# Kernel optimization log

Measured on AMD Instinct MI355X. Metric: run time of the kernel, lower is better.

The kernel has to match this reference:

```python
import jax, jax.numpy as jnp
import numpy as np

N, E = 50000, 800000
D_IN, D_HID, D_OUT = 128, 128, 64
BN_EPS = 1e-5
GEN_EPS = 1e-7


def _lin_init(k, fan_in, shape):
    lim = 1.0 / np.sqrt(fan_in)
    return jax.random.uniform(k, shape, minval=-lim, maxval=lim, dtype=jnp.float32)


def setup_inputs() -> dict:
    key = jax.random.key(0)
    ks = jax.random.split(key, 12)
    x = jax.random.normal(ks[0], (N, D_IN), dtype=jnp.float32)
    edge_index = jax.random.randint(ks[1], (2, E), 0, N, dtype=jnp.int64)
    return {
        "x": x,
        # GCNConv 0 and 1 (Glorot-ish uniform init like PyG Linear)
        "W0": _lin_init(ks[2], D_IN, (D_IN, D_HID)), "b0": jnp.zeros((D_HID,), jnp.float32),
        "g0": jnp.ones((D_HID,), jnp.float32), "beta0": jnp.zeros((D_HID,), jnp.float32),
        "W1": _lin_init(ks[3], D_HID, (D_HID, D_HID)), "b1": jnp.zeros((D_HID,), jnp.float32),
        "g1": jnp.ones((D_HID,), jnp.float32), "beta1": jnp.zeros((D_HID,), jnp.float32),
        # GENConv MLP: [D_HID] -> [2*D_HID] (BN+ReLU) -> [D_OUT]
        "Wg1": _lin_init(ks[4], D_HID, (D_HID, 2 * D_HID)), "bg1": jnp.zeros((2 * D_HID,), jnp.float32),
        "gg": jnp.ones((2 * D_HID,), jnp.float32), "betag": jnp.zeros((2 * D_HID,), jnp.float32),
        "Wg2": _lin_init(ks[5], 2 * D_HID, (2 * D_HID, D_OUT)), "bg2": jnp.zeros((D_OUT,), jnp.float32),
        "edge_index": edge_index,
    }


def _bn(h, gamma, beta):
    # BatchNorm1d, training-mode batch statistics (biased variance)
    mu = jnp.mean(h, axis=0)
    var = jnp.mean(jnp.square(h - mu), axis=0)
    return (h - mu) * jax.lax.rsqrt(var + BN_EPS) * gamma + beta


def _gcn_conv(x, W, b, src, dst, n):
    # GCNConv: D^-1/2 (A + I) D^-1/2 (x W) + b
    loop = jnp.arange(n, dtype=src.dtype)
    s = jnp.concatenate([src, loop])
    d = jnp.concatenate([dst, loop])
    deg = jax.ops.segment_sum(jnp.ones_like(s, dtype=x.dtype), d, num_segments=n)
    dinv = jax.lax.rsqrt(deg)  # deg >= 1 due to self-loops
    norm = dinv[s] * dinv[d]   # [E+N]
    h = x @ W                  # [N, D]
    agg = jax.ops.segment_sum(norm[:, None] * h[s], d, num_segments=n)
    return agg + b


def _gen_conv(x, W1, b1, g, beta, W2, b2, src, dst, n):
    # GENConv (defaults): msg = relu(x_j) + eps; per-channel softmax aggregation
    # (t=1); residual add of x_dst; then MLP [D, 2D (BN+ReLU), D_out].
    msg = jax.nn.relu(x[src]) + GEN_EPS            # [E, D]
    m = jax.ops.segment_max(msg, dst, num_segments=n)
    m = jnp.where(jnp.isfinite(m), m, 0.0)         # guard zero in-degree nodes
    ex = jnp.exp(msg - m[dst])                     # [E, D]
    denom = jax.ops.segment_sum(ex, dst, num_segments=n)
    num = jax.ops.segment_sum(ex * msg, dst, num_segments=n)
    agg = num / jnp.maximum(denom, 1e-16)          # [N, D]
    out = agg + x                                  # residual
    h = jax.nn.relu(_bn(out @ W1 + b1, g, beta))
    return h @ W2 + b2


def reference(x, W0, b0, g0, beta0, W1, b1, g1, beta1,
              Wg1, bg1, gg, betag, Wg2, bg2, edge_index):
    src, dst = edge_index[0], edge_index[1]
    n = x.shape[0]
    # layer 0: GCNConv -> BN -> ReLU (dropout is identity in eval)
    h = _gcn_conv(x, W0, b0, src, dst, n)
    h = jax.nn.relu(_bn(h, g0, beta0))
    # layer 1
    h = _gcn_conv(h, W1, b1, src, dst, n)
    h = jax.nn.relu(_bn(h, g1, beta1))
    # final GENConv + log-softmax over classes
    h = _gen_conv(h, Wg1, bg1, gg, betag, Wg2, bg2, src, dst, n)
    return jax.nn.log_softmax(h, axis=-1)
```

## Files before the change

### kernel.cpp

```cpp
#include <hip/hip_runtime.h>
#include <hip/hip_bf16.h>

#define DIN 128
#define DHID 128
#define DCLS 64
#define BN_EPS 1e-5f
#define GEN_EPS 1e-7f

typedef __attribute__((ext_vector_type(8))) short short8;
typedef __attribute__((ext_vector_type(4))) float f32x4;

static __device__ __forceinline__ float bf2f(unsigned short u) {
    union { float f; unsigned int i; } x; x.i = ((unsigned int)u) << 16; return x.f;
}
static __device__ __forceinline__ unsigned short f2bf(float f) {
    union { float f; unsigned int i; } x; x.f = f;
    unsigned int r = x.i + 0x7fffu + ((x.i >> 16) & 1u);
    return (unsigned short)(r >> 16);
}
static __device__ __forceinline__ float bflo(unsigned int u) {
    union { float f; unsigned int i; } x; x.i = u << 16; return x.f;
}
static __device__ __forceinline__ float bfhi(unsigned int u) {
    union { float f; unsigned int i; } x; x.i = u & 0xffff0000u; return x.f;
}
static __device__ __forceinline__ unsigned int packbf(float lo, float hi) {
    return ((unsigned int)f2bf(hi) << 16) | f2bf(lo);
}

__global__ void k_hist(const int* __restrict__ dst, int* __restrict__ counts, int E) {
    int e = blockIdx.x * 256 + threadIdx.x;
    if (e < E) atomicAdd(&counts[dst[e]], 1);
}

__global__ __launch_bounds__(256) void k_scan1(const int* __restrict__ counts,
        int* __restrict__ roff, int* __restrict__ bsum, int N) {
    __shared__ int ls[256];
    int t = threadIdx.x;
    int base = blockIdx.x * 1024 + t * 4;
    int c0 = 0, c1 = 0, c2 = 0, c3 = 0;
    if (base + 3 < N) {
        int4 v = *(const int4*)(counts + base);
        c0 = v.x; c1 = v.y; c2 = v.z; c3 = v.w;
    } else {
        if (base + 0 < N) c0 = counts[base + 0];
        if (base + 1 < N) c1 = counts[base + 1];
        if (base + 2 < N) c2 = counts[base + 2];
        if (base + 3 < N) c3 = counts[base + 3];
    }
    ls[t] = c0 + c1 + c2 + c3;
    __syncthreads();
    for (int off = 1; off < 256; off <<= 1) {
        int v = (t >= off) ? ls[t - off] : 0;
        __syncthreads();
        ls[t] += v;
        __syncthreads();
    }
    int r = (t == 0) ? 0 : ls[t - 1];
    if (base + 0 < N) { roff[base + 0] = r; r += c0; }
    if (base + 1 < N) { roff[base + 1] = r; r += c1; }
    if (base + 2 < N) { roff[base + 2] = r; r += c2; }
    if (base + 3 < N) { roff[base + 3] = r; }
    if (t == 255) bsum[blockIdx.x] = ls[255];
}

__global__ __launch_bounds__(1024) void k_scan2(int* __restrict__ bsum, int nblk) {
    __shared__ int ls[1024];
    int t = threadIdx.x;
    ls[t] = (t < nblk) ? bsum[t] : 0;
    __syncthreads();
    for (int off = 1; off < 1024; off <<= 1) {
        int v = (t >= off) ? ls[t - off] : 0;
        __syncthreads();
        ls[t] += v;
        __syncthreads();
    }
    if (t < nblk) bsum[t] = (t == 0) ? 0 : ls[t - 1];
}

__global__ void k_scan3(const int* __restrict__ counts, const int* __restrict__ bsum,
        int* __restrict__ roff, int* __restrict__ cursor, float* __restrict__ dinv,
        int N, int E) {
    int i = blockIdx.x * 256 + threadIdx.x;
    if (i < N) {
        int r = roff[i] + bsum[i >> 10];
        roff[i] = r; cursor[i] = r;
        dinv[i] = rsqrtf((float)(counts[i] + 1));
    }
    if (i == 0) roff[N] = E;
}

__global__ void k_fill(const int* __restrict__ src, const int* __restrict__ dst,
        int* __restrict__ cursor, int* __restrict__ srcs, int E) {
    int e = blockIdx.x * 256 + threadIdx.x;
    if (e < E) {
        int d = dst[e];
        int p = atomicAdd(&cursor[d], 1);
        srcs[p] = src[e];
    }
}

__global__ void k_wt(const float* __restrict__ W, unsigned short* __restrict__ Wt, int K, int Dout) {
    int i = blockIdx.x * 256 + threadIdx.x;
    if (i >= K * Dout) return;
    int n = i / K, k = i - n * K;
    Wt[i] = f2bf(W[(size_t)k * Dout + n]);
}

template<int K, bool ABF16, bool OBF16>
__global__ __launch_bounds__(256) void k_gemm(const void* __restrict__ Av,
        const unsigned short* __restrict__ Wt, const float* __restrict__ bias,
        const float* __restrict__ scale, const float* __restrict__ shift,
        const float* __restrict__ rowscale,
        void* __restrict__ Cv, int nrows, int Dout) {
    constexpr int KP = K + 8;
    __shared__ unsigned short sA[64 * KP];
    __shared__ unsigned short sW[64 * KP];
    const int tid = threadIdx.x;
    const int row0 = blockIdx.x * 64, col0 = blockIdx.y * 64;

#pragma unroll
    for (int it = 0; it < (64 * K) / (256 * 4); ++it) {
        int idx = (it * 256 + tid) * 4;
        int r = idx / K, c = idx % K;
        int gr = row0 + r;
        float v0 = 0.f, v1 = 0.f, v2 = 0.f, v3 = 0.f;
        if (gr < nrows) {
            if (ABF16) {
                ushort4 u = *(const ushort4*)((const unsigned short*)Av + (size_t)gr * K + c);
                v0 = bf2f(u.x); v1 = bf2f(u.y); v2 = bf2f(u.z); v3 = bf2f(u.w);
            } else {
                float4 f = *(const float4*)((const float*)Av + (size_t)gr * K + c);
                v0 = f.x; v1 = f.y; v2 = f.z; v3 = f.w;
            }
            if (scale) {
                v0 = fmaxf(v0 * scale[c + 0] + shift[c + 0], 0.f);
                v1 = fmaxf(v1 * scale[c + 1] + shift[c + 1], 0.f);
                v2 = fmaxf(v2 * scale[c + 2] + shift[c + 2], 0.f);
                v3 = fmaxf(v3 * scale[c + 3] + shift[c + 3], 0.f);
            }
        }
        ushort4 o; o.x = f2bf(v0); o.y = f2bf(v1); o.z = f2bf(v2); o.w = f2bf(v3);
        *(ushort4*)(&sA[r * KP + c]) = o;
    }
#pragma unroll
    for (int it = 0; it < (64 * K) / (256 * 8); ++it) {
        int idx = (it * 256 + tid) * 8;
        int r = idx / K, c = idx % K;
        uint4 u = *(const uint4*)(Wt + (size_t)(col0 + r) * K + c);
        *(uint4*)(&sW[r * KP + c]) = u;
    }
    __syncthreads();

    const int w = tid >> 6, lane = tid & 63;
    const int wr = (w >> 1) * 32, wc = (w & 1) * 32;
    const int lr = lane & 15, kg = (lane >> 4) * 8;
    f32x4 acc[2][2] = {};
#pragma unroll
    for (int kk = 0; kk < K; kk += 32) {
        short8 af[2], bfr[2];
#pragma unroll
        for (int mi = 0; mi < 2; mi++)
            af[mi] = *(const short8*)(&sA[(wr + mi * 16 + lr) * KP + kk + kg]);
#pragma unroll
        for (int ni = 0; ni < 2; ni++)
            bfr[ni] = *(const short8*)(&sW[(wc + ni * 16 + lr) * KP + kk + kg]);
#pragma unroll
        for (int mi = 0; mi < 2; mi++)
#pragma unroll
            for (int ni = 0; ni < 2; ni++)
                acc[mi][ni] = __builtin_amdgcn_mfma_f32_16x16x32_bf16(af[mi], bfr[ni], acc[mi][ni], 0, 0, 0);
    }
#pragma unroll
    for (int mi = 0; mi < 2; mi++) {
#pragma unroll
        for (int ni = 0; ni < 2; ni++) {
            int r = wr + mi * 16 + (lane >> 4) * 4;
            int cgl = col0 + wc + ni * 16 + (lane & 15);
            float bv = bias ? bias[cgl] : 0.f;
#pragma unroll
            for (int j = 0; j < 4; j++) {
                int gr = row0 + r + j;
                if (gr < nrows) {
                    float val = acc[mi][ni][j] + bv;
                    if (rowscale) val *= rowscale[gr];
                    if (OBF16) ((unsigned short*)Cv)[(size_t)gr * Dout + cgl] = f2bf(val);
                    else       ((float*)Cv)[(size_t)gr * Dout + cgl] = val;
                }
            }
        }
    }
}

__global__ __launch_bounds__(256) void k_gcn_agg(const unsigned short* __restrict__ p,
        const int* __restrict__ roff, const int* __restrict__ srcs,
        const float* __restrict__ dinv, const float* __restrict__ b,
        unsigned short* __restrict__ out, int N) {
    int nw = (gridDim.x * 256) >> 6;
    int wid = (blockIdx.x * 256 + threadIdx.x) >> 6;
    int lane = threadIdx.x & 63;
    int q = lane >> 4, l16 = lane & 15;
    int c = l16 * 8;
    float4 bl = *(const float4*)(b + c);
    float4 bh = *(const float4*)(b + c + 4);
    for (int d = wid; d < N; d += nw) {
        float a0=0.f,a1=0.f,a2=0.f,a3=0.f,a4=0.f,a5=0.f,a6=0.f,a7=0.f;
        int e0 = roff[d], e1 = roff[d + 1];
        for (int e = e0 + q; e < e1; e += 4) {
            int s = srcs[e];
            uint4 u = ((const uint4*)(p + (size_t)s * 128))[l16];
            a0 += bflo(u.x); a1 += bfhi(u.x);
            a2 += bflo(u.y); a3 += bfhi(u.y);
            a4 += bflo(u.z); a5 += bfhi(u.z);
            a6 += bflo(u.w); a7 += bfhi(u.w);
        }
        if (q == 0) {
            uint4 u = ((const uint4*)(p + (size_t)d * 128))[l16];
            a0 += bflo(u.x); a1 += bfhi(u.x);
            a2 += bflo(u.y); a3 += bfhi(u.y);
            a4 += bflo(u.z); a5 += bfhi(u.z);
            a6 += bflo(u.w); a7 += bfhi(u.w);
        }
        a0 += __shfl_xor(a0,16); a0 += __shfl_xor(a0,32);
        a1 += __shfl_xor(a1,16); a1 += __shfl_xor(a1,32);
        a2 += __shfl_xor(a2,16); a2 += __shfl_xor(a2,32);
        a3 += __shfl_xor(a3,16); a3 += __shfl_xor(a3,32);
        a4 += __shfl_xor(a4,16); a4 += __shfl_xor(a4,32);
        a5 += __shfl_xor(a5,16); a5 += __shfl_xor(a5,32);
        a6 += __shfl_xor(a6,16); a6 += __shfl_xor(a6,32);
        a7 += __shfl_xor(a7,16); a7 += __shfl_xor(a7,32);
        if (q == 0) {
            float dv = dinv[d];
            uint4 o;
            o.x = packbf(dv*a0 + bl.x, dv*a1 + bl.y);
            o.y = packbf(dv*a2 + bl.z, dv*a3 + bl.w);
            o.z = packbf(dv*a4 + bh.x, dv*a5 + bh.y);
            o.w = packbf(dv*a6 + bh.z, dv*a7 + bh.w);
            ((uint4*)(out + (size_t)d * 128))[l16] = o;
        }
    }
}

__global__ __launch_bounds__(256) void k_gen_agg(const unsigned short* __restrict__ t4,
        const int* __restrict__ roff, const int* __restrict__ srcs,
        const float* __restrict__ scale, const float* __restrict__ shift,
        unsigned short* __restrict__ out, int N) {
    int nw = (gridDim.x * 256) >> 6;
    int wid = (blockIdx.x * 256 + threadIdx.x) >> 6;
    int lane = threadIdx.x & 63;
    int q = lane >> 4, l16 = lane & 15;
    int c = l16 * 8;
    float4 scl = *(const float4*)(scale + c);
    float4 sch = *(const float4*)(scale + c + 4);
    float4 shl = *(const float4*)(shift + c);
    float4 shh = *(const float4*)(shift + c + 4);
    float sc[8] = {scl.x, scl.y, scl.z, scl.w, sch.x, sch.y, sch.z, sch.w};
    float sh[8] = {shl.x, shl.y, shl.z, shl.w, shh.x, shh.y, shh.z, shh.w};
    for (int d = wid; d < N; d += nw) {
        float de[8] = {0,0,0,0,0,0,0,0};
        float nu[8] = {0,0,0,0,0,0,0,0};
        int e0 = roff[d], e1 = roff[d + 1];
        for (int e = e0 + q; e < e1; e += 4) {
            int s = srcs[e];
            uint4 u = ((const uint4*)(t4 + (size_t)s * 128))[l16];
            float v[8] = {bflo(u.x), bfhi(u.x), bflo(u.y), bfhi(u.y),
                          bflo(u.z), bfhi(u.z), bflo(u.w), bfhi(u.w)};
#pragma unroll
            for (int k = 0; k < 8; k++) {
                float m = fmaxf(v[k] * sc[k] + sh[k], 0.f) + GEN_EPS;
                float w = __expf(fminf(m, 80.f));
                de[k] += w; nu[k] += w * m;
            }
        }
#pragma unroll
        for (int k = 0; k < 8; k++) {
            de[k] += __shfl_xor(de[k],16); de[k] += __shfl_xor(de[k],32);
            nu[k] += __shfl_xor(nu[k],16); nu[k] += __shfl_xor(nu[k],32);
        }
        if (q == 0) {
            uint4 u = ((const uint4*)(t4 + (size_t)d * 128))[l16];
            float v[8] = {bflo(u.x), bfhi(u.x), bflo(u.y), bfhi(u.y),
                          bflo(u.z), bfhi(u.z), bflo(u.w), bfhi(u.w)};
            float r[8];
            bool has = (e1 > e0);
#pragma unroll
            for (int k = 0; k < 8; k++) {
                float h2 = fmaxf(v[k] * sc[k] + sh[k], 0.f);
                float a = has ? nu[k] / de[k] : 0.f;
                r[k] = a + h2;
            }
            uint4 o;
            o.x = packbf(r[0], r[1]); o.y = packbf(r[2], r[3]);
            o.z = packbf(r[4], r[5]); o.w = packbf(r[6], r[7]);
            ((uint4*)(out + (size_t)d * 128))[l16] = o;
        }
    }
}

template<int D>
__global__ __launch_bounds__(256) void k_stats(const unsigned short* __restrict__ h,
        float* __restrict__ gsum, float* __restrict__ gsq, int N) {
    constexpr int HC = D / 2, TPC = 256 / HC;
    int t = threadIdx.x;
    int cp = t % HC, slot = t / HC;
    int c = cp * 2;
    float s0 = 0.f, s1 = 0.f, q0 = 0.f, q1 = 0.f;
    for (int node = blockIdx.x * TPC + slot; node < N; node += gridDim.x * TPC) {
        ushort2 u = *(const ushort2*)(h + (size_t)node * D + c);
        float v0 = bf2f(u.x), v1 = bf2f(u.y);
        s0 += v0; s1 += v1; q0 += v0 * v0; q1 += v1 * v1;
    }
    __shared__ float red[256 * 4];
    red[t * 4] = s0; red[t * 4 + 1] = s1; red[t * 4 + 2] = q0; red[t * 4 + 3] = q1;
    __syncthreads();
    if (slot == 0) {
        for (int k2 = 1; k2 < TPC; k2++) {
            int o = (t + k2 * HC) * 4;
            s0 += red[o]; s1 += red[o + 1]; q0 += red[o + 2]; q1 += red[o + 3];
        }
        atomicAdd(&gsum[c], s0); atomicAdd(&gsum[c + 1], s1);
        atomicAdd(&gsq[c], q0); atomicAdd(&gsq[c + 1], q1);
    }
}

__global__ void k_fin(const float* __restrict__ sum, const float* __restrict__ sq,
        const float* __restrict__ g, const float* __restrict__ beta,
        float* __restrict__ scale, float* __restrict__ shift, int D, float invN) {
    int c = threadIdx.x;
    if (c < D) {
        float mu = sum[c] * invN;
        float var = sq[c] * invN - mu * mu;
        float s = g[c] * rsqrtf(var + BN_EPS);
        scale[c] = s;
        shift[c] = beta[c] - mu * s;
    }
}

__global__ __launch_bounds__(256) void k_head(float* __restrict__ out, int N) {
    int wid = blockIdx.x * 4 + (threadIdx.x >> 6);
    int lane = threadIdx.x & 63;
    if (wid >= N) return;
    float v = out[(size_t)wid * 64 + lane];
    float m = v;
    for (int o = 32; o; o >>= 1) m = fmaxf(m, __shfl_xor(m, o));
    float e = __expf(v - m);
    float s = e;
    for (int o = 32; o; o >>= 1) s += __shfl_xor(s, o);
    out[(size_t)wid * 64 + lane] = v - m - __logf(s);
}

extern "C" void kernel_launch(void* const* d_in, const int* in_sizes, int n_in,
                              void* d_out, int out_size, void* d_ws, size_t ws_size,
                              hipStream_t stream) {
    const float* x   = (const float*)d_in[0];
    const float* W0  = (const float*)d_in[1];
    const float* b0  = (const float*)d_in[2];
    const float* g0  = (const float*)d_in[3];
    const float* be0 = (const float*)d_in[4];
    const float* W1  = (const float*)d_in[5];
    const float* b1  = (const float*)d_in[6];
    const float* g1  = (const float*)d_in[7];
    const float* be1 = (const float*)d_in[8];
    const float* Wg1 = (const float*)d_in[9];
    const float* bg1 = (const float*)d_in[10];
    const float* gg  = (const float*)d_in[11];
    const float* beg = (const float*)d_in[12];
    const float* Wg2 = (const float*)d_in[13];
    const float* bg2 = (const float*)d_in[14];
    const int*   ei  = (const int*)d_in[15];

    const int N = in_sizes[0] / DIN;
    const int E = in_sizes[15] / 2;
    const int* src = ei;
    const int* dst = ei + E;

    char* ws = (char*)d_ws;
    size_t off = 0;
    auto alloc = [&](size_t b) { size_t o = off; off = (off + b + 255) & ~(size_t)255; return o; };
    size_t o_counts = alloc((size_t)N * 4);
    size_t o_stats  = alloc(1024 * 4);
    size_t o_cursor = alloc((size_t)N * 4);
    size_t o_roff   = alloc(((size_t)N + 1) * 4);
    size_t o_srcs   = alloc((size_t)E * 4);
    size_t o_dinv   = alloc((size_t)N * 4);
    size_t o_bsum   = alloc(1024 * 4);
    size_t o_ss     = alloc(1024 * 4);
    size_t o_w0t    = alloc(128 * 128 * 2);
    size_t o_w1t    = alloc(128 * 128 * 2);
    size_t o_wg1t   = alloc(256 * 128 * 2);
    size_t o_wg2t   = alloc(64 * 256 * 2);
    size_t o_xa     = alloc((size_t)N * 128 * 2);
    size_t o_xb     = alloc((size_t)N * 128 * 2);
    size_t o_c      = alloc((size_t)N * 256 * 2);
    (void)ws_size; (void)n_in; (void)out_size;

    int* counts = (int*)(ws + o_counts);
    float* stats = (float*)(ws + o_stats);
    int* cursor = (int*)(ws + o_cursor);
    int* roff = (int*)(ws + o_roff);
    int* srcs = (int*)(ws + o_srcs);
    float* dinv = (float*)(ws + o_dinv);
    int* bsum = (int*)(ws + o_bsum);
    float* ssz = (float*)(ws + o_ss);
    unsigned short* w0t  = (unsigned short*)(ws + o_w0t);
    unsigned short* w1t  = (unsigned short*)(ws + o_w1t);
    unsigned short* wg1t = (unsigned short*)(ws + o_wg1t);
    unsigned short* wg2t = (unsigned short*)(ws + o_wg2t);
    unsigned short* xa = (unsigned short*)(ws + o_xa);
    unsigned short* xb = (unsigned short*)(ws + o_xb);
    unsigned short* cb = (unsigned short*)(ws + o_c);

    float* sum0 = stats;       float* sq0 = stats + 128;
    float* sum1 = stats + 256; float* sq1 = stats + 384;
    float* sumg = stats + 512; float* sqg = stats + 768;
    float* scale0 = ssz;       float* shift0 = ssz + 128;
    float* scale1 = ssz + 256; float* shift1 = ssz + 384;
    float* scaleg = ssz + 512; float* shiftg = ssz + 768;

    hipMemsetAsync(ws + o_counts, 0, o_cursor - o_counts, stream);

    int egrid = (E + 255) / 256;
    int nblk = (N + 1023) / 1024;
    k_hist<<<egrid, 256, 0, stream>>>(dst, counts, E);
    k_scan1<<<nblk, 256, 0, stream>>>(counts, roff, bsum, N);
    k_scan2<<<1, 1024, 0, stream>>>(bsum, nblk);
    k_scan3<<<(N + 255) / 256, 256, 0, stream>>>(counts, bsum, roff, cursor, dinv, N, E);
    k_fill<<<egrid, 256, 0, stream>>>(src, dst, cursor, srcs, E);

    k_wt<<<(128 * 128 + 255) / 256, 256, 0, stream>>>(W0, w0t, 128, 128);
    k_wt<<<(128 * 128 + 255) / 256, 256, 0, stream>>>(W1, w1t, 128, 128);
    k_wt<<<(128 * 256 + 255) / 256, 256, 0, stream>>>(Wg1, wg1t, 128, 256);
    k_wt<<<(256 * 64 + 255) / 256, 256, 0, stream>>>(Wg2, wg2t, 256, 64);

    int rb = (N + 63) / 64;
    const float invN = 1.f / (float)N;

    k_gemm<128, false, true><<<dim3(rb, 2), 256, 0, stream>>>(x, w0t, nullptr, nullptr, nullptr, dinv, xa, N, 128);
    k_gcn_agg<<<2048, 256, 0, stream>>>(xa, roff, srcs, dinv, b0, xb, N);
    k_stats<128><<<1024, 256, 0, stream>>>(xb, sum0, sq0, N);
    k_fin<<<1, 256, 0, stream>>>(sum0, sq0, g0, be0, scale0, shift0, 128, invN);

    k_gemm<128, true, true><<<dim3(rb, 2), 256, 0, stream>>>(xb, w1t, nullptr, scale0, shift0, dinv, xa, N, 128);
    k_gcn_agg<<<2048, 256, 0, stream>>>(xa, roff, srcs, dinv, b1, xb, N);
    k_stats<128><<<1024, 256, 0, stream>>>(xb, sum1, sq1, N);
    k_fin<<<1, 256, 0, stream>>>(sum1, sq1, g1, be1, scale1, shift1, 128, invN);

    k_gen_agg<<<2048, 256, 0, stream>>>(xb, roff, srcs, scale1, shift1, xa, N);

    k_gemm<128, true, true><<<dim3(rb, 4), 256, 0, stream>>>(xa, wg1t, bg1, nullptr, nullptr, nullptr, cb, N, 256);
    k_stats<256><<<1024, 256, 0, stream>>>(cb, sumg, sqg, N);
    k_fin<<<1, 256, 0, stream>>>(sumg, sqg, gg, beg, scaleg, shiftg, 256, invN);
    k_gemm<256, true, false><<<dim3(rb, 1), 256, 0, stream>>>(cb, wg2t, bg2, scaleg, shiftg, nullptr, d_out, N, 64);

    k_head<<<(N + 3) / 4, 256, 0, stream>>>((float*)d_out, N);
}
```

Measured before the change: 524.8 us.

## Fuse BN stats into GCN aggregation and precompute per-node softmax weights

The GCN aggregation kernel now accumulates per-channel sum and sum-of-squares of its output and atomically adds them to global stats, replacing two separate k_stats passes over the node features. A new k_genpre kernel computes exp(m) and exp(m)*m once per node into a bf16 table (reusing the cb buffer). k_gen_agg then gathers these precomputed values instead of recomputing the BN affine, ReLU and exp for every edge. This doubles the bytes gathered per edge in the GEN aggregation and adds bf16 rounding of the weights, while removing per-edge transcendental work. Dropping the segment max is safe here only because the exponent is clamped at 80.

```diff
diff --git a/kernel.cpp b/kernel.cpp
--- a/kernel.cpp
+++ b/kernel.cpp
@@ -195,7 +195,8 @@
 __global__ __launch_bounds__(256) void k_gcn_agg(const unsigned short* __restrict__ p,
         const int* __restrict__ roff, const int* __restrict__ srcs,
         const float* __restrict__ dinv, const float* __restrict__ b,
-        unsigned short* __restrict__ out, int N) {
+        unsigned short* __restrict__ out,
+        float* __restrict__ gsum, float* __restrict__ gsq, int N) {
     int nw = (gridDim.x * 256) >> 6;
     int wid = (blockIdx.x * 256 + threadIdx.x) >> 6;
     int lane = threadIdx.x & 63;
@@ -203,6 +204,9 @@
     int c = l16 * 8;
     float4 bl = *(const float4*)(b + c);
     float4 bh = *(const float4*)(b + c + 4);
+    float bb[8] = {bl.x, bl.y, bl.z, bl.w, bh.x, bh.y, bh.z, bh.w};
+    float ls[8] = {0,0,0,0,0,0,0,0};
+    float lq[8] = {0,0,0,0,0,0,0,0};
     for (int d = wid; d < N; d += nw) {
         float a0=0.f,a1=0.f,a2=0.f,a3=0.f,a4=0.f,a5=0.f,a6=0.f,a7=0.f;
         int e0 = roff[d], e1 = roff[d + 1];
@@ -231,17 +235,73 @@
         a7 += __shfl_xor(a7,16); a7 += __shfl_xor(a7,32);
         if (q == 0) {
             float dv = dinv[d];
+            float r0 = dv*a0 + bb[0], r1 = dv*a1 + bb[1];
+            float r2 = dv*a2 + bb[2], r3 = dv*a3 + bb[3];
+            float r4 = dv*a4 + bb[4], r5 = dv*a5 + bb[5];
+            float r6 = dv*a6 + bb[6], r7 = dv*a7 + bb[7];
+            ls[0]+=r0; lq[0]+=r0*r0; ls[1]+=r1; lq[1]+=r1*r1;
+            ls[2]+=r2; lq[2]+=r2*r2; ls[3]+=r3; lq[3]+=r3*r3;
+            ls[4]+=r4; lq[4]+=r4*r4; ls[5]+=r5; lq[5]+=r5*r5;
+            ls[6]+=r6; lq[6]+=r6*r6; ls[7]+=r7; lq[7]+=r7*r7;
             uint4 o;
-            o.x = packbf(dv*a0 + bl.x, dv*a1 + bl.y);
-            o.y = packbf(dv*a2 + bl.z, dv*a3 + bl.w);
-            o.z = packbf(dv*a4 + bh.x, dv*a5 + bh.y);
-            o.w = packbf(dv*a6 + bh.z, dv*a7 + bh.w);
+            o.x = packbf(r0, r1); o.y = packbf(r2, r3);
+            o.z = packbf(r4, r5); o.w = packbf(r6, r7);
             ((uint4*)(out + (size_t)d * 128))[l16] = o;
         }
     }
+    __shared__ float sred[4][128];
+    __shared__ float qred[4][128];
+    int wv = threadIdx.x >> 6;
+    if (q == 0) {
+#pragma unroll
+        for (int k = 0; k < 8; k++) { sred[wv][c + k] = ls[k]; qred[wv][c + k] = lq[k]; }
+    }
+    __syncthreads();
+    int t = threadIdx.x;
+    if (t < 128) {
+        float s = sred[0][t] + sred[1][t] + sred[2][t] + sred[3][t];
+        float qq = qred[0][t] + qred[1][t] + qred[2][t] + qred[3][t];
+        atomicAdd(&gsum[t], s);
+        atomicAdd(&gsq[t], qq);
+    }
+}
+
+__global__ __launch_bounds__(256) void k_genpre(const unsigned short* __restrict__ t4,
+        const float* __restrict__ scale, const float* __restrict__ shift,
+        unsigned short* __restrict__ wt, int N) {
+    int i = blockIdx.x * 256 + threadIdx.x;
+    int node = i >> 4, l16 = i & 15;
+    if (node >= N) return;
+    int c = l16 * 8;
+    float4 scl = *(const float4*)(scale + c);
+    float4 sch = *(const float4*)(scale + c + 4);
+    float4 shl = *(const float4*)(shift + c);
+    float4 shh = *(const float4*)(shift + c + 4);
+    float sc[8] = {scl.x, scl.y, scl.z, scl.w, sch.x, sch.y, sch.z, sch.w};
+    float sh[8] = {shl.x, shl.y, shl.z, shl.w, shh.x, shh.y, shh.z, shh.w};
+    uint4 u = ((const uint4*)(t4 + (size_t)node * 128))[l16];
+    float v[8] = {bflo(u.x), bfhi(u.x), bflo(u.y), bfhi(u.y),
+                  bflo(u.z), bfhi(u.z), bflo(u.w), bfhi(u.w)};
+    float w[8], wm[8];
+#pragma unroll
+    for (int k = 0; k < 8; k++) {
+        float m = fmaxf(v[k] * sc[k] + sh[k], 0.f) + GEN_EPS;
+        m = fminf(m, 80.f);
+        w[k] = __expf(m);
+        wm[k] = w[k] * m;
+    }
+    uint4* row = (uint4*)(wt + (size_t)node * 256);
+    uint4 ow, om;
+    ow.x = packbf(w[0], w[1]); ow.y = packbf(w[2], w[3]);
+    ow.z = packbf(w[4], w[5]); ow.w = packbf(w[6], w[7]);
+    om.x = packbf(wm[0], wm[1]); om.y = packbf(wm[2], wm[3]);
+    om.z = packbf(wm[4], wm[5]); om.w = packbf(wm[6], wm[7]);
+    row[l16] = ow;
+    row[16 + l16] = om;
 }
 
 __global__ __launch_bounds__(256) void k_gen_agg(const unsigned short* __restrict__ t4,
+        const unsigned short* __restrict__ wt,
         const int* __restrict__ roff, const int* __restrict__ srcs,
         const float* __restrict__ scale, const float* __restrict__ shift,
         unsigned short* __restrict__ out, int N) {
@@ -250,27 +310,23 @@
     int lane = threadIdx.x & 63;
     int q = lane >> 4, l16 = lane & 15;
     int c = l16 * 8;
-    float4 scl = *(const float4*)(scale + c);
-    float4 sch = *(const float4*)(scale + c + 4);
-    float4 shl = *(const float4*)(shift + c);
-    float4 shh = *(const float4*)(shift + c + 4);
-    float sc[8] = {scl.x, scl.y, scl.z, scl.w, sch.x, sch.y, sch.z, sch.w};
-    float sh[8] = {shl.x, shl.y, shl.z, shl.w, shh.x, shh.y, shh.z, shh.w};
     for (int d = wid; d < N; d += nw) {
         float de[8] = {0,0,0,0,0,0,0,0};
         float nu[8] = {0,0,0,0,0,0,0,0};
         int e0 = roff[d], e1 = roff[d + 1];
         for (int e = e0 + q; e < e1; e += 4) {
             int s = srcs[e];
-            uint4 u = ((const uint4*)(t4 + (size_t)s * 128))[l16];
-            float v[8] = {bflo(u.x), bfhi(u.x), bflo(u.y), bfhi(u.y),
-                          bflo(u.z), bfhi(u.z), bflo(u.w), bfhi(u.w)};
-#pragma unroll
-            for (int k = 0; k < 8; k++) {
-                float m = fmaxf(v[k] * sc[k] + sh[k], 0.f) + GEN_EPS;
-                float w = __expf(fminf(m, 80.f));
-                de[k] += w; nu[k] += w * m;
-            }
+            const uint4* row = (const uint4*)(wt + (size_t)s * 256);
+            uint4 uw = row[l16];
+            uint4 um = row[16 + l16];
+            de[0] += bflo(uw.x); de[1] += bfhi(uw.x);
+            de[2] += bflo(uw.y); de[3] += bfhi(uw.y);
+            de[4] += bflo(uw.z); de[5] += bfhi(uw.z);
+            de[6] += bflo(uw.w); de[7] += bfhi(uw.w);
+            nu[0] += bflo(um.x); nu[1] += bfhi(um.x);
+            nu[2] += bflo(um.y); nu[3] += bfhi(um.y);
+            nu[4] += bflo(um.z); nu[5] += bfhi(um.z);
+            nu[6] += bflo(um.w); nu[7] += bfhi(um.w);
         }
 #pragma unroll
         for (int k = 0; k < 8; k++) {
@@ -278,6 +334,12 @@
             nu[k] += __shfl_xor(nu[k],16); nu[k] += __shfl_xor(nu[k],32);
         }
         if (q == 0) {
+            float4 scl = *(const float4*)(scale + c);
+            float4 sch = *(const float4*)(scale + c + 4);
+            float4 shl = *(const float4*)(shift + c);
+            float4 shh = *(const float4*)(shift + c + 4);
+            float sc[8] = {scl.x, scl.y, scl.z, scl.w, sch.x, sch.y, sch.z, sch.w};
+            float sh[8] = {shl.x, shl.y, shl.z, shl.w, shh.x, shh.y, shh.z, shh.w};
             uint4 u = ((const uint4*)(t4 + (size_t)d * 128))[l16];
             float v[8] = {bflo(u.x), bfhi(u.x), bflo(u.y), bfhi(u.y),
                           bflo(u.z), bfhi(u.z), bflo(u.w), bfhi(u.w)};
@@ -409,6 +471,7 @@
     unsigned short* xa = (unsigned short*)(ws + o_xa);
     unsigned short* xb = (unsigned short*)(ws + o_xb);
     unsigned short* cb = (unsigned short*)(ws + o_c);
+    unsigned short* wtab = cb;
 
     float* sum0 = stats;       float* sq0 = stats + 128;
     float* sum1 = stats + 256; float* sq1 = stats + 384;
@@ -436,16 +499,15 @@
     const float invN = 1.f / (float)N;
 
     k_gemm<128, false, true><<<dim3(rb, 2), 256, 0, stream>>>(x, w0t, nullptr, nullptr, nullptr, dinv, xa, N, 128);
-    k_gcn_agg<<<2048, 256, 0, stream>>>(xa, roff, srcs, dinv, b0, xb, N);
-    k_stats<128><<<1024, 256, 0, stream>>>(xb, sum0, sq0, N);
+    k_gcn_agg<<<2048, 256, 0, stream>>>(xa, roff, srcs, dinv, b0, xb, sum0, sq0, N);
     k_fin<<<1, 256, 0, stream>>>(sum0, sq0, g0, be0, scale0, shift0, 128, invN);
 
     k_gemm<128, true, true><<<dim3(rb, 2), 256, 0, stream>>>(xb, w1t, nullptr, scale0, shift0, dinv, xa, N, 128);
-    k_gcn_agg<<<2048, 256, 0, stream>>>(xa, roff, srcs, dinv, b1, xb, N);
-    k_stats<128><<<1024, 256, 0, stream>>>(xb, sum1, sq1, N);
+    k_gcn_agg<<<2048, 256, 0, stream>>>(xa, roff, srcs, dinv, b1, xb, sum1, sq1, N);
     k_fin<<<1, 256, 0, stream>>>(sum1, sq1, g1, be1, scale1, shift1, 128, invN);
 
-    k_gen_agg<<<2048, 256, 0, stream>>>(xb, roff, srcs, scale1, shift1, xa, N);
+    k_genpre<<<(N * 16 + 255) / 256, 256, 0, stream>>>(xb, scale1, shift1, wtab, N);
+    k_gen_agg<<<2048, 256, 0, stream>>>(xb, wtab, roff, srcs, scale1, shift1, xa, N);
 
     k_gemm<128, true, true><<<dim3(rb, 4), 256, 0, stream>>>(xa, wg1t, bg1, nullptr, nullptr, nullptr, cb, N, 256);
     k_stats<256><<<1024, 256, 0, stream>>>(cb, sumg, sqg, N);
```

Result: faster. 499.9 us (-4.7%).
